# Performance work log

Measured on AMD Instinct MI355X. Metric: run time of the kernel, lower is better.

## Reference

```python
import jax, jax.numpy as jnp
import numpy as np

H, DK = 16, 64
F = H * DK  # n_feat = 1024
B, T = 2, 2048


def setup_inputs() -> dict:
    key = jax.random.key(0)
    ks = jax.random.split(key, 11)
    mk = lambda k, sh: jax.random.normal(k, sh, dtype=jnp.float32)
    inp = {
        "query": mk(ks[0], (B, T, F)),
        "key": mk(ks[1], (B, T, F)),
        "value": mk(ks[2], (B, T, F)),
    }
    # Standard RoPE frequency table, shaped [T,1,1,DK] to broadcast over [t,b,h,d].
    pos = jnp.arange(T, dtype=jnp.float32)[:, None]
    inv_freq = 1.0 / (10000.0 ** (jnp.arange(0, DK, 2, dtype=jnp.float32) / DK))
    ang = pos * inv_freq                       # [T, DK/2]
    emb = jnp.concatenate([ang, ang], axis=-1)  # [T, DK]
    inp["cos"] = jnp.cos(emb)[:, None, None, :]
    inp["sin"] = jnp.sin(emb)[:, None, None, :]
    scale = 1.0 / np.sqrt(F).astype(np.float32)
    for i, n in enumerate(["wq", "wk", "wv", "wo"]):
        inp[n] = mk(ks[3 + i], (F, F)) * scale  # torch Linear weight layout [out,in]
    for i, n in enumerate(["bq", "bk", "bv", "bo"]):
        inp[n] = mk(ks[7 + i], (F,)) * 0.01
    return inp


def _rtt_half(x):
    d = x.shape[-1]
    return jnp.concatenate([-x[..., d // 2:], x[..., :d // 2]], axis=-1)


def reference(query, key, value, cos, sin, wq, bq, wk, bk, wv, bv, wo, bo):
    b, t, f = query.shape
    h, d = H, DK
    # [b,t,f] -> [t,b,h,d] as in the torch code (RoPE applied pre-projection)
    to_tbhd = lambda x: jnp.swapaxes(x, 0, 1).reshape(t, b, h, d)
    q = to_tbhd(query)
    k = to_tbhd(key)
    c, s = cos[:t], sin[:t]
    q = q * c + _rtt_half(q) * s
    k = k * c + _rtt_half(k) * s
    back = lambda x: jnp.swapaxes(x.reshape(t, b, f), 0, 1)  # -> [b,t,f]
    q, k = back(q), back(k)
    lin = lambda x, w, bias: x @ w.T + bias
    Q = lin(q, wq, bq).reshape(b, t, h, d)
    K = lin(k, wk, bk).reshape(b, t, h, d)
    V = lin(value, wv, bv).reshape(b, t, h, d)
    scores = jnp.einsum('bqhd,bkhd->bhqk', Q, K) / jnp.sqrt(jnp.float32(d))
    attn = jax.nn.softmax(scores, axis=-1)
    o = jnp.einsum('bhqk,bkhd->bqhd', attn, V).reshape(b, t, f)
    return o @ wo.T + bo
```

## Files before the change

kernel.cpp:

```cpp
#include <hip/hip_runtime.h>
#include <hip/hip_bf16.h>

#define DEVI __device__ __forceinline__

typedef unsigned short u16;
typedef unsigned int u32;
typedef __attribute__((ext_vector_type(8))) short bf16x8;
typedef __attribute__((ext_vector_type(4))) short bf16x4;
typedef __attribute__((ext_vector_type(4))) float f32x4;

#define Bn 2
#define Tn 2048
#define Hn 16
#define Dn 64
#define Fn 1024

DEVI u16 tobf(float f) {
    __hip_bfloat16 h = __float2bfloat16(f);
    return __builtin_bit_cast(u16, h);
}
DEVI float frombf(u16 u) {
    return __builtin_bit_cast(float, ((u32)u) << 16);
}

DEVI f32x4 mfma16(bf16x8 a, bf16x8 b, f32x4 c) {
    return __builtin_amdgcn_mfma_f32_16x16x32_bf16(a, b, c, 0, 0, 0);
}

DEVI void gload_lds16(const u16* g, u16* l) {
    __builtin_amdgcn_global_load_lds(
        (const __attribute__((address_space(1))) void*)g,
        (__attribute__((address_space(3))) void*)l, 16, 0, 0);
}

__global__ __launch_bounds__(256) void k_prep(const float* __restrict__ q,
                                              const float* __restrict__ k,
                                              const float* __restrict__ v,
                                              const float* __restrict__ cosb,
                                              const float* __restrict__ sinb,
                                              const float* __restrict__ wq,
                                              const float* __restrict__ wk,
                                              const float* __restrict__ wv,
                                              const float* __restrict__ wo,
                                              u16* __restrict__ Aq,
                                              u16* __restrict__ Ak,
                                              u16* __restrict__ Av) {
    if (blockIdx.x < 4096) {
        unsigned idx = blockIdx.x * 256 + threadIdx.x;
        unsigned which = idx >> 19;
        unsigned r = idx & 0x7FFFFu;
        unsigned d0 = (r & 7u) << 2;
        unsigned h = (r >> 3) & 15u;
        unsigned t = (r >> 7) & 2047u;
        unsigned b = (r >> 18) & 1u;
        const float* src = which ? k : q;
        u16* dst = which ? Ak : Aq;
        size_t base = ((size_t)(b * Tn + t)) * Fn + h * Dn;
        float4 lo = *(const float4*)(src + base + d0);
        float4 hi = *(const float4*)(src + base + d0 + 32);
        float4 cl = *(const float4*)(cosb + (size_t)t * Dn + d0);
        float4 ch = *(const float4*)(cosb + (size_t)t * Dn + d0 + 32);
        float4 sl = *(const float4*)(sinb + (size_t)t * Dn + d0);
        float4 sh = *(const float4*)(sinb + (size_t)t * Dn + d0 + 32);
        bf16x4 olo, ohi;
        olo[0] = (short)tobf(lo.x * cl.x - hi.x * sl.x);
        olo[1] = (short)tobf(lo.y * cl.y - hi.y * sl.y);
        olo[2] = (short)tobf(lo.z * cl.z - hi.z * sl.z);
        olo[3] = (short)tobf(lo.w * cl.w - hi.w * sl.w);
        ohi[0] = (short)tobf(hi.x * ch.x + lo.x * sh.x);
        ohi[1] = (short)tobf(hi.y * ch.y + lo.y * sh.y);
        ohi[2] = (short)tobf(hi.z * ch.z + lo.z * sh.z);
        ohi[3] = (short)tobf(hi.w * ch.w + lo.w * sh.w);
        *(bf16x4*)(dst + base + d0) = olo;
        *(bf16x4*)(dst + base + d0 + 32) = ohi;
    } else {
        size_t i8 = (((size_t)blockIdx.x - 4096) * 256 + threadIdx.x) * 8;
        const size_t M4 = (size_t)4 << 20, M1 = (size_t)1 << 20;
        const float* src;
        size_t off;
        if (i8 < M4)              { src = v;  off = i8; }
        else if (i8 < M4 + M1)    { src = wq; off = i8 - M4; }
        else if (i8 < M4 + 2*M1)  { src = wk; off = i8 - M4 - M1; }
        else if (i8 < M4 + 3*M1)  { src = wv; off = i8 - M4 - 2*M1; }
        else                      { src = wo; off = i8 - M4 - 3*M1; }
        float4 a = *(const float4*)(src + off);
        float4 c = *(const float4*)(src + off + 4);
        bf16x8 vv;
        vv[0] = (short)tobf(a.x); vv[1] = (short)tobf(a.y);
        vv[2] = (short)tobf(a.z); vv[3] = (short)tobf(a.w);
        vv[4] = (short)tobf(c.x); vv[5] = (short)tobf(c.y);
        vv[6] = (short)tobf(c.z); vv[7] = (short)tobf(c.w);
        *(bf16x8*)(Av + i8) = vv;
    }
}

DEVI void store_out(u16* p, float v) { *p = tobf(v); }
DEVI void store_out(float* p, float v) { *p = v; }

template <typename OUT>
DEVI void gemm_body(const u16* __restrict__ A, const u16* __restrict__ W,
                    const float* __restrict__ bias, OUT* __restrict__ C,
                    float scale, u16* As, u16* Bs, int mode) {
    const int tid = threadIdx.x;
    const int lane = tid & 63;
    const int wave = tid >> 6;
    const int l15 = lane & 15, l4 = lane >> 4;
    const int bm = blockIdx.y << 7, bn = blockIdx.x << 7;
    const int wr = (wave >> 1) << 6, wc = (wave & 1) << 6;

    const int c0 = tid, c1 = tid + 256;
    const u16* A0p = A + (size_t)(bm + (c0 >> 2)) * 1024 + ((c0 & 3) << 3);
    const u16* A1p = A + (size_t)(bm + (c1 >> 2)) * 1024 + ((c1 & 3) << 3);
    const u16* B0p = W + (size_t)(bn + (c0 >> 2)) * 1024 + ((c0 & 3) << 3);
    const u16* B1p = W + (size_t)(bn + (c1 >> 2)) * 1024 + ((c1 & 3) << 3);
    u16* Ad0 = As + (c0 << 3);
    u16* Ad1 = As + (c1 << 3);
    u16* Bd0 = Bs + (c0 << 3);
    u16* Bd1 = Bs + (c1 << 3);

    f32x4 acc[4][4] = {};

    for (int k0 = 0; k0 < 1024; k0 += 32) {
        gload_lds16(A0p + k0, Ad0);
        gload_lds16(A1p + k0, Ad1);
        gload_lds16(B0p + k0, Bd0);
        gload_lds16(B1p + k0, Bd1);
        __syncthreads();
        bf16x8 af[4], bfr[4];
        #pragma unroll
        for (int m = 0; m < 4; m++)
            af[m] = *(const bf16x8*)(As + (wr + m * 16 + l15) * 32 + (l4 << 3));
        #pragma unroll
        for (int n = 0; n < 4; n++)
            bfr[n] = *(const bf16x8*)(Bs + (wc + n * 16 + l15) * 32 + (l4 << 3));
        #pragma unroll
        for (int m = 0; m < 4; m++)
            #pragma unroll
            for (int n = 0; n < 4; n++)
                acc[m][n] = mfma16(af[m], bfr[n], acc[m][n]);
        __syncthreads();
    }

    #pragma unroll
    for (int m = 0; m < 4; m++)
        #pragma unroll
        for (int n = 0; n < 4; n++) {
            const int gcol = bn + wc + n * 16 + l15;
            const float bb = bias[gcol];
            #pragma unroll
            for (int j = 0; j < 4; j++) {
                const int grow = bm + wr + m * 16 + (l4 << 2) + j;
                const float val = (acc[m][n][j] + bb) * scale;
                if (mode == 0) {
                    store_out(C + (size_t)grow * 1024 + gcol, val);
                } else {
                    const int b = grow >> 11, t = grow & 2047;
                    const int h = gcol >> 6, d = gcol & 63;
                    const int bh = b * 16 + h, tt2 = t >> 6, r = t & 63;
                    const size_t tbase = ((size_t)(bh * 32 + tt2)) << 12;
                    size_t off;
                    if (mode == 1) {
                        const int nn = ((r >> 5) << 1) | ((r >> 2) & 1);
                        const int kk = d >> 5, ll4 = (d >> 3) & 3, e = d & 7;
                        const int ll15 = (((r >> 3) & 3) << 2) | (r & 3);
                        off = tbase + ((size_t)(nn * 2 + kk) << 9) +
                              ((ll4 * 16 + ll15) << 3) + e;
                    } else {
                        const int kk = r >> 5, ll4 = (r >> 3) & 3, e = r & 7;
                        const int nd = d >> 4, ll15 = d & 15;
                        off = tbase + ((size_t)(kk * 4 + nd) << 9) +
                              ((ll4 * 16 + ll15) << 3) + e;
                    }
                    ((u16*)C)[off] = tobf(val);
                }
            }
        }
}

__global__ __launch_bounds__(256) void k_gemm_qkv(
    const u16* A0, const u16* W0, const float* b0, u16* C0,
    const u16* A1, const u16* W1, const float* b1, u16* C1,
    const u16* A2, const u16* W2, const float* b2, u16* C2) {
    __shared__ __align__(16) u16 As[128 * 32];
    __shared__ __align__(16) u16 Bs[128 * 32];
    const int z = blockIdx.z;
    const u16* A = z == 0 ? A0 : (z == 1 ? A1 : A2);
    const u16* W = z == 0 ? W0 : (z == 1 ? W1 : W2);
    const float* bias = z == 0 ? b0 : (z == 1 ? b1 : b2);
    u16* C = z == 0 ? C0 : (z == 1 ? C1 : C2);
    const float scale = z == 0 ? 0.125f * 1.4426950408889634f : 1.0f;
    gemm_body<u16>(A, W, bias, C, scale, As, Bs, z);
}

__global__ __launch_bounds__(256) void k_gemm_f32(const u16* __restrict__ A,
                                                  const u16* __restrict__ W,
                                                  const float* __restrict__ bias,
                                                  float* __restrict__ C) {
    __shared__ __align__(16) u16 As[128 * 32];
    __shared__ __align__(16) u16 Bs[128 * 32];
    gemm_body<float>(A, W, bias, C, 1.0f, As, Bs, 0);
}

__global__ __launch_bounds__(256) void k_attn(const u16* __restrict__ Qp,
                                              const u16* __restrict__ Kr,
                                              const u16* __restrict__ Vr,
                                              u16* __restrict__ Op0,
                                              u16* __restrict__ Op1,
                                              u16* __restrict__ Op2,
                                              u16* __restrict__ Op3,
                                              float* __restrict__ Ls) {
    __shared__ __align__(16) u16 Ks[2][4096];
    __shared__ __align__(16) u16 Vs[2][4096];
    const int tid = threadIdx.x, wave = tid >> 6, lane = tid & 63;
    const int l15 = lane & 15, l4 = lane >> 4;
    const int bh = blockIdx.x, b = bh >> 4, h = bh & 15;
    const int sp = blockIdx.z;
    const int q0 = blockIdx.y * 128 + wave * 32;
    const int tbase = sp << 3;

    bf16x8 aq[2][2];
    #pragma unroll
    for (int mq = 0; mq < 2; mq++)
        #pragma unroll
        for (int kk = 0; kk < 2; kk++)
            aq[mq][kk] = *(const bf16x8*)(Qp +
                ((size_t)(b * Tn + q0 + mq * 16 + l15)) * Fn + h * Dn + kk * 32 + (l4 << 3));

    f32x4 o[2][4] = {};
    float lrun[2] = {0.f, 0.f};
    const f32x4 zero4 = {0.f, 0.f, 0.f, 0.f};

    bf16x8 ones;
    #pragma unroll
    for (int j = 0; j < 8; j++) ones[j] = (short)0x3F80;

    const u16* Kbr = Kr + ((size_t)bh << 17);
    const u16* Vbr = Vr + ((size_t)bh << 17);
    const int lo8 = lane * 8;

    #define STAGE(bf, tg)                                                     \
        _Pragma("unroll")                                                     \
        for (int i = 0; i < 2; i++) {                                         \
            const int c = wave + i * 4;                                       \
            gload_lds16(Kbr + (((tg) * 8 + c) << 9) + lo8,                    \
                        &Ks[bf][(c << 9) + lo8]);                             \
            gload_lds16(Vbr + (((tg) * 8 + c) << 9) + lo8,                    \
                        &Vs[bf][(c << 9) + lo8]);                             \
        }

    STAGE(0, tbase);
    __syncthreads();
    int cur = 0;

    #pragma unroll 1
    for (int tt = 0; tt < 8; tt++) {
        if (tt < 7) STAGE(cur ^ 1, tbase + tt + 1);

        bf16x8 ka[4][2], va[2][4];
        #pragma unroll
        for (int n = 0; n < 4; n++)
            #pragma unroll
            for (int kk = 0; kk < 2; kk++)
                ka[n][kk] = *(const bf16x8*)(&Ks[cur][((n * 2 + kk) << 9) + lo8]);
        #pragma unroll
        for (int kk = 0; kk < 2; kk++)
            #pragma unroll
            for (int nd = 0; nd < 4; nd++)
                va[kk][nd] = *(const bf16x8*)(&Vs[cur][((kk * 4 + nd) << 9) + lo8]);

        f32x4 s[2][4];
        __builtin_amdgcn_s_setprio(1);
        #pragma unroll
        for (int n = 0; n < 4; n++) {
            s[0][n] = mfma16(ka[n][0], aq[0][0], zero4);
            s[1][n] = mfma16(ka[n][0], aq[1][0], zero4);
            s[0][n] = mfma16(ka[n][1], aq[0][1], s[0][n]);
            s[1][n] = mfma16(ka[n][1], aq[1][1], s[1][n]);
        }
        __builtin_amdgcn_s_setprio(0);

        bf16x8 pb[2][2];
        #pragma unroll
        for (int mq = 0; mq < 2; mq++)
            #pragma unroll
            for (int kk = 0; kk < 2; kk++) {
                float p0 = __builtin_amdgcn_exp2f(s[mq][2 * kk][0]);
                float p1 = __builtin_amdgcn_exp2f(s[mq][2 * kk][1]);
                float p2 = __builtin_amdgcn_exp2f(s[mq][2 * kk][2]);
                float p3 = __builtin_amdgcn_exp2f(s[mq][2 * kk][3]);
                float p4 = __builtin_amdgcn_exp2f(s[mq][2 * kk + 1][0]);
                float p5 = __builtin_amdgcn_exp2f(s[mq][2 * kk + 1][1]);
                float p6 = __builtin_amdgcn_exp2f(s[mq][2 * kk + 1][2]);
                float p7 = __builtin_amdgcn_exp2f(s[mq][2 * kk + 1][3]);
                bf16x8 pv;
                pv[0] = (short)tobf(p0); pv[1] = (short)tobf(p1);
                pv[2] = (short)tobf(p2); pv[3] = (short)tobf(p3);
                pv[4] = (short)tobf(p4); pv[5] = (short)tobf(p5);
                pv[6] = (short)tobf(p6); pv[7] = (short)tobf(p7);
                pb[mq][kk] = pv;
            }

        __builtin_amdgcn_s_setprio(1);
        f32x4 osum0 = mfma16(ones, pb[0][0], zero4);
        f32x4 osum1 = mfma16(ones, pb[1][0], zero4);
        osum0 = mfma16(ones, pb[0][1], osum0);
        osum1 = mfma16(ones, pb[1][1], osum1);
        #pragma unroll
        for (int kk = 0; kk < 2; kk++)
            #pragma unroll
            for (int nd = 0; nd < 4; nd++) {
                o[0][nd] = mfma16(va[kk][nd], pb[0][kk], o[0][nd]);
                o[1][nd] = mfma16(va[kk][nd], pb[1][kk], o[1][nd]);
            }
        __builtin_amdgcn_s_setprio(0);
        lrun[0] += osum0[0];
        lrun[1] += osum1[0];

        __syncthreads();
        cur ^= 1;
    }
    #undef STAGE

    u16* OpS = sp == 0 ? Op0 : (sp == 1 ? Op1 : (sp == 2 ? Op2 : Op3));
    #pragma unroll
    for (int mq = 0; mq < 2; mq++) {
        const int q = q0 + mq * 16 + l15;
        float inv = 1.f / lrun[mq];
        #pragma unroll
        for (int nd = 0; nd < 4; nd++) {
            bf16x4 ov;
            ov[0] = (short)tobf(o[mq][nd][0] * inv);
            ov[1] = (short)tobf(o[mq][nd][1] * inv);
            ov[2] = (short)tobf(o[mq][nd][2] * inv);
            ov[3] = (short)tobf(o[mq][nd][3] * inv);
            *(bf16x4*)(OpS + ((size_t)(b * Tn + q)) * Fn +
                       h * Dn + nd * 16 + (l4 << 2)) = ov;
        }
        if (l4 == 0)
            Ls[(((size_t)(sp * 2 + b)) * Tn + q) * Hn + h] = lrun[mq];
    }
}

__global__ __launch_bounds__(256) void k_combine(const u16* __restrict__ Op0,
                                                 const u16* __restrict__ Op1,
                                                 const u16* __restrict__ Op2,
                                                 const u16* __restrict__ Op3,
                                                 const float* __restrict__ Ls,
                                                 u16* __restrict__ Oa) {
    size_t e0 = ((size_t)blockIdx.x * 256 + threadIdx.x) * 8;
    int row = (int)(e0 >> 10);
    int b = row >> 11, q = row & 2047;
    int h = (int)(e0 >> 6) & 15;
    float l0 = Ls[(((size_t)(0 + b)) * Tn + q) * Hn + h];
    float l1 = Ls[(((size_t)(2 + b)) * Tn + q) * Hn + h];
    float l2 = Ls[(((size_t)(4 + b)) * Tn + q) * Hn + h];
    float l3 = Ls[(((size_t)(6 + b)) * Tn + q) * Hn + h];
    float inv = 1.f / (l0 + l1 + l2 + l3);
    float w0 = l0 * inv, w1 = l1 * inv, w2 = l2 * inv, w3 = l3 * inv;
    bf16x8 x0 = *(const bf16x8*)(Op0 + e0);
    bf16x8 x1 = *(const bf16x8*)(Op1 + e0);
    bf16x8 x2 = *(const bf16x8*)(Op2 + e0);
    bf16x8 x3 = *(const bf16x8*)(Op3 + e0);
    bf16x8 out;
    #pragma unroll
    for (int j = 0; j < 8; j++)
        out[j] = (short)tobf(frombf((u16)x0[j]) * w0 + frombf((u16)x1[j]) * w1 +
                             frombf((u16)x2[j]) * w2 + frombf((u16)x3[j]) * w3);
    *(bf16x8*)(Oa + e0) = out;
}

extern "C" void kernel_launch(void* const* d_in, const int* in_sizes, int n_in,
                              void* d_out, int out_size, void* d_ws, size_t ws_size,
                              hipStream_t stream) {
    const float* q    = (const float*)d_in[0];
    const float* k    = (const float*)d_in[1];
    const float* v    = (const float*)d_in[2];
    const float* cosb = (const float*)d_in[3];
    const float* sinb = (const float*)d_in[4];
    const float* wq   = (const float*)d_in[5];
    const float* wk   = (const float*)d_in[6];
    const float* wv   = (const float*)d_in[7];
    const float* wo   = (const float*)d_in[8];
    const float* bq   = (const float*)d_in[9];
    const float* bk   = (const float*)d_in[10];
    const float* bv   = (const float*)d_in[11];
    const float* bo   = (const float*)d_in[12];

    char* ws = (char*)d_ws;
    char* dob = (char*)d_out;
    const size_t MB = (size_t)1 << 20;
    u16* Aq  = (u16*)(ws);
    u16* Ak  = (u16*)(ws + 8 * MB);
    u16* Av  = (u16*)(ws + 16 * MB);
    u16* Wq  = (u16*)(ws + 24 * MB);
    u16* Wk  = (u16*)(ws + 26 * MB);
    u16* Wv  = (u16*)(ws + 28 * MB);
    u16* Wo  = (u16*)(ws + 30 * MB);
    u16* Qp  = (u16*)(ws + 32 * MB);
    u16* Kr  = (u16*)(ws + 40 * MB);
    u16* Vr  = (u16*)(ws + 48 * MB);
    u16* Op0 = (u16*)(dob);
    u16* Op1 = (u16*)(dob + 8 * MB);
    u16* Op2 = (u16*)(ws);
    u16* Op3 = (u16*)(ws + 8 * MB);
    float* Ls = (float*)(ws + 16 * MB);
    u16* Oa  = (u16*)(ws);

    k_prep<<<8192, 256, 0, stream>>>(q, k, v, cosb, sinb, wq, wk, wv, wo,
                                     Aq, Ak, Av);
    k_gemm_qkv<<<dim3(8, 32, 3), 256, 0, stream>>>(Aq, Wq, bq, Qp,
                                                   Ak, Wk, bk, Kr,
                                                   Av, Wv, bv, Vr);
    k_attn<<<dim3(32, 16, 4), 256, 0, stream>>>(Qp, Kr, Vr, Op0, Op1, Op2, Op3, Ls);
    k_combine<<<2048, 256, 0, stream>>>(Op0, Op1, Op2, Op3, Ls, Oa);
    k_gemm_f32<<<dim3(8, 32), 256, 0, stream>>>(Oa, Wo, bo, (float*)d_out);
}
```

Measured before the change: 139.3 us.

## Halve attention KV splits, accumulate row sums in MFMA, swizzle GEMM tiles

The attention kernel now splits the key range into 2 chunks instead of 4, so each block walks 16 tiles and writes half as many partial outputs. The combine kernel therefore reads only two partial buffers. Row sums now accumulate directly in the MFMA accumulator across iterations instead of in scalar adds. The GEMM blocks also get a swizzled tile mapping meant to improve L2 reuse of the A rows. The trade-off is fewer attention blocks (1024), which lowers parallelism and lengthens each block's serial loop.

```diff
diff --git a/kernel.cpp b/kernel.cpp
--- a/kernel.cpp
+++ b/kernel.cpp
@@ -105,7 +105,9 @@
     const int lane = tid & 63;
     const int wave = tid >> 6;
     const int l15 = lane & 15, l4 = lane >> 4;
-    const int bm = blockIdx.y << 7, bn = blockIdx.x << 7;
+    const int id = blockIdx.x + (blockIdx.y << 3);
+    const int swz = ((id & 7) << 5) + (id >> 3);
+    const int bn = (swz & 7) << 7, bm = (swz >> 3) << 7;
     const int wr = (wave >> 1) << 6, wc = (wave & 1) << 6;
 
     const int c0 = tid, c1 = tid + 256;
@@ -206,8 +208,6 @@
                                               const u16* __restrict__ Vr,
                                               u16* __restrict__ Op0,
                                               u16* __restrict__ Op1,
-                                              u16* __restrict__ Op2,
-                                              u16* __restrict__ Op3,
                                               float* __restrict__ Ls) {
     __shared__ __align__(16) u16 Ks[2][4096];
     __shared__ __align__(16) u16 Vs[2][4096];
@@ -216,7 +216,7 @@
     const int bh = blockIdx.x, b = bh >> 4, h = bh & 15;
     const int sp = blockIdx.z;
     const int q0 = blockIdx.y * 128 + wave * 32;
-    const int tbase = sp << 3;
+    const int tbase = sp << 4;
 
     bf16x8 aq[2][2];
     #pragma unroll
@@ -227,7 +227,7 @@
                 ((size_t)(b * Tn + q0 + mq * 16 + l15)) * Fn + h * Dn + kk * 32 + (l4 << 3));
 
     f32x4 o[2][4] = {};
-    float lrun[2] = {0.f, 0.f};
+    f32x4 osum[2] = {};
     const f32x4 zero4 = {0.f, 0.f, 0.f, 0.f};
 
     bf16x8 ones;
@@ -253,8 +253,8 @@
     int cur = 0;
 
     #pragma unroll 1
-    for (int tt = 0; tt < 8; tt++) {
-        if (tt < 7) STAGE(cur ^ 1, tbase + tt + 1);
+    for (int tt = 0; tt < 16; tt++) {
+        if (tt < 15) STAGE(cur ^ 1, tbase + tt + 1);
 
         bf16x8 ka[4][2], va[2][4];
         #pragma unroll
@@ -301,10 +301,10 @@
             }
 
         __builtin_amdgcn_s_setprio(1);
-        f32x4 osum0 = mfma16(ones, pb[0][0], zero4);
-        f32x4 osum1 = mfma16(ones, pb[1][0], zero4);
-        osum0 = mfma16(ones, pb[0][1], osum0);
-        osum1 = mfma16(ones, pb[1][1], osum1);
+        osum[0] = mfma16(ones, pb[0][0], osum[0]);
+        osum[1] = mfma16(ones, pb[1][0], osum[1]);
+        osum[0] = mfma16(ones, pb[0][1], osum[0]);
+        osum[1] = mfma16(ones, pb[1][1], osum[1]);
         #pragma unroll
         for (int kk = 0; kk < 2; kk++)
             #pragma unroll
@@ -313,19 +313,18 @@
                 o[1][nd] = mfma16(va[kk][nd], pb[1][kk], o[1][nd]);
             }
         __builtin_amdgcn_s_setprio(0);
-        lrun[0] += osum0[0];
-        lrun[1] += osum1[0];
 
         __syncthreads();
         cur ^= 1;
     }
     #undef STAGE
 
-    u16* OpS = sp == 0 ? Op0 : (sp == 1 ? Op1 : (sp == 2 ? Op2 : Op3));
+    u16* OpS = sp ? Op1 : Op0;
     #pragma unroll
     for (int mq = 0; mq < 2; mq++) {
         const int q = q0 + mq * 16 + l15;
-        float inv = 1.f / lrun[mq];
+        const float lsum = osum[mq][0];
+        float inv = 1.f / lsum;
         #pragma unroll
         for (int nd = 0; nd < 4; nd++) {
             bf16x4 ov;
@@ -337,14 +336,12 @@
                        h * Dn + nd * 16 + (l4 << 2)) = ov;
         }
         if (l4 == 0)
-            Ls[(((size_t)(sp * 2 + b)) * Tn + q) * Hn + h] = lrun[mq];
+            Ls[(((size_t)(sp * 2 + b)) * Tn + q) * Hn + h] = lsum;
     }
 }
 
 __global__ __launch_bounds__(256) void k_combine(const u16* __restrict__ Op0,
                                                  const u16* __restrict__ Op1,
-                                                 const u16* __restrict__ Op2,
-                                                 const u16* __restrict__ Op3,
                                                  const float* __restrict__ Ls,
                                                  u16* __restrict__ Oa) {
     size_t e0 = ((size_t)blockIdx.x * 256 + threadIdx.x) * 8;
@@ -353,19 +350,14 @@
     int h = (int)(e0 >> 6) & 15;
     float l0 = Ls[(((size_t)(0 + b)) * Tn + q) * Hn + h];
     float l1 = Ls[(((size_t)(2 + b)) * Tn + q) * Hn + h];
-    float l2 = Ls[(((size_t)(4 + b)) * Tn + q) * Hn + h];
-    float l3 = Ls[(((size_t)(6 + b)) * Tn + q) * Hn + h];
-    float inv = 1.f / (l0 + l1 + l2 + l3);
-    float w0 = l0 * inv, w1 = l1 * inv, w2 = l2 * inv, w3 = l3 * inv;
+    float inv = 1.f / (l0 + l1);
+    float w0 = l0 * inv, w1 = l1 * inv;
     bf16x8 x0 = *(const bf16x8*)(Op0 + e0);
     bf16x8 x1 = *(const bf16x8*)(Op1 + e0);
-    bf16x8 x2 = *(const bf16x8*)(Op2 + e0);
-    bf16x8 x3 = *(const bf16x8*)(Op3 + e0);
     bf16x8 out;
     #pragma unroll
     for (int j = 0; j < 8; j++)
-        out[j] = (short)tobf(frombf((u16)x0[j]) * w0 + frombf((u16)x1[j]) * w1 +
-                             frombf((u16)x2[j]) * w2 + frombf((u16)x3[j]) * w3);
+        out[j] = (short)tobf(frombf((u16)x0[j]) * w0 + frombf((u16)x1[j]) * w1);
     *(bf16x8*)(Oa + e0) = out;
 }
 
@@ -401,8 +393,6 @@
     u16* Vr  = (u16*)(ws + 48 * MB);
     u16* Op0 = (u16*)(dob);
     u16* Op1 = (u16*)(dob + 8 * MB);
-    u16* Op2 = (u16*)(ws);
-    u16* Op3 = (u16*)(ws + 8 * MB);
     float* Ls = (float*)(ws + 16 * MB);
     u16* Oa  = (u16*)(ws);
 
@@ -411,7 +401,7 @@
     k_gemm_qkv<<<dim3(8, 32, 3), 256, 0, stream>>>(Aq, Wq, bq, Qp,
                                                    Ak, Wk, bk, Kr,
                                                    Av, Wv, bv, Vr);
-    k_attn<<<dim3(32, 16, 4), 256, 0, stream>>>(Qp, Kr, Vr, Op0, Op1, Op2, Op3, Ls);
-    k_combine<<<2048, 256, 0, stream>>>(Op0, Op1, Op2, Op3, Ls, Oa);
+    k_attn<<<dim3(32, 16, 2), 256, 0, stream>>>(Qp, Kr, Vr, Op0, Op1, Ls);
+    k_combine<<<2048, 256, 0, stream>>>(Op0, Op1, Ls, Oa);
     k_gemm_f32<<<dim3(8, 32), 256, 0, stream>>>(Oa, Wo, bo, (float*)d_out);
 }
```

Measured after the change: 129.3 us. 1.08x faster.
